# Kernel tuning notes

Hardware: AMD Instinct MI355X
Metric: run time of the kernel (lower is better)

The kernel has to match this reference:

```python
import jax, jax.numpy as jnp
import numpy as np

B, H, W = 4, 64, 64
INPLANES, PLANES, G, K = 608, 152, 19, 3
KK = K * K
EPS = 1e-5


def conv2d(x, w, stride=1, padding=0, dilation=1):
    return jax.lax.conv_general_dilated(
        x, w, (stride, stride), [(padding, padding)] * 2,
        rhs_dilation=(dilation, dilation),
        dimension_numbers=("NCHW", "OIHW", "NCHW"))


def bn(x, g, b, m, v):
    # inference-mode batchnorm (affine with running stats)
    inv = g / jnp.sqrt(v + EPS)
    return x * inv[None, :, None, None] + (b - m * inv)[None, :, None, None]


def deform_conv(x, offset, w, pad=1, dil=1):
    # x: [B,C,H,W], offset: [B, 2*G*KK, H, W] ((dy,dx) pairs per group per tap), w: [Cout,C,K,K]
    Bs, C, Hh, Ww = x.shape
    Cg = C // G
    off = offset.reshape(Bs, G, KK, 2, Hh, Ww)
    ky, kx = jnp.meshgrid(jnp.arange(K), jnp.arange(K), indexing="ij")
    base_y = (jnp.arange(Hh) - pad)[None, None, None, :, None] + (dil * ky.reshape(-1))[None, None, :, None, None]
    base_x = (jnp.arange(Ww) - pad)[None, None, None, None, :] + (dil * kx.reshape(-1))[None, None, :, None, None]
    ys = base_y + off[:, :, :, 0]  # [B,G,KK,H,W]
    xs = base_x + off[:, :, :, 1]
    y0 = jnp.floor(ys)
    x0 = jnp.floor(xs)
    wy = ys - y0
    wx = xs - x0
    y0i = y0.astype(jnp.int32)
    x0i = x0.astype(jnp.int32)
    xf = x.reshape(Bs, G, Cg, Hh * Ww)

    def gather(yi, xi, wgt):
        valid = ((yi >= 0) & (yi < Hh) & (xi >= 0) & (xi < Ww)).astype(x.dtype)
        idx = jnp.clip(yi, 0, Hh - 1) * Ww + jnp.clip(xi, 0, Ww - 1)
        idxf = jnp.broadcast_to(idx.reshape(Bs, G, 1, KK * Hh * Ww), (Bs, G, Cg, KK * Hh * Ww))
        g = jnp.take_along_axis(xf, idxf, axis=3).reshape(Bs, G, Cg, KK, Hh, Ww)
        return g * (wgt * valid)[:, :, None]

    samp = (gather(y0i, x0i, (1 - wy) * (1 - wx))
            + gather(y0i, x0i + 1, (1 - wy) * wx)
            + gather(y0i + 1, x0i, wy * (1 - wx))
            + gather(y0i + 1, x0i + 1, wy * wx))  # [B,G,Cg,KK,H,W]
    wr = w.reshape(w.shape[0], G, Cg, KK)
    return jnp.einsum("bgckhw,ogck->bohw", samp, wr)


def setup_inputs() -> dict:
    key = jax.random.key(0)
    ks = jax.random.split(key, 8)
    d = {}
    d["x"] = jax.random.normal(ks[0], (B, INPLANES, H, W), jnp.float32)
    d["conv1_w"] = jax.random.normal(ks[1], (PLANES, INPLANES, 1, 1), jnp.float32) * 0.05
    d["conv2_w"] = jax.random.normal(ks[2], (2 * G * KK, PLANES, 3, 3), jnp.float32) * 0.01
    d["dconv_w"] = jax.random.normal(ks[3], (PLANES, PLANES, 3, 3), jnp.float32) * 0.05
    d["conv3_w"] = jax.random.normal(ks[4], (4 * PLANES, PLANES, 1, 1), jnp.float32) * 0.05
    for i, (name, c) in enumerate([("bn1", PLANES), ("bn2", PLANES), ("bn3", 4 * PLANES)]):
        k1, k2, k3, k4 = jax.random.split(ks[5 + i], 4)
        d[name + "_g"] = jax.random.uniform(k1, (c,), jnp.float32, 0.5, 1.5)
        d[name + "_b"] = jax.random.normal(k2, (c,), jnp.float32) * 0.1
        d[name + "_m"] = jax.random.normal(k3, (c,), jnp.float32) * 0.1
        d[name + "_v"] = jax.random.uniform(k4, (c,), jnp.float32, 0.5, 1.5)
    return d


def reference(x, conv1_w, conv2_w, dconv_w, conv3_w,
              bn1_g, bn1_b, bn1_m, bn1_v,
              bn2_g, bn2_b, bn2_m, bn2_v,
              bn3_g, bn3_b, bn3_m, bn3_v):
    out = jax.nn.relu(conv2d(x, conv1_w))           # conv1 -> relu (order as in source)
    out = bn(out, bn1_g, bn1_b, bn1_m, bn1_v)       # -> bn1
    offset = conv2d(out, conv2_w, padding=1)         # offset-generating 3x3 conv
    out = deform_conv(out, offset, dconv_w)          # deformable 3x3 conv
    out = bn(jax.nn.relu(out), bn2_g, bn2_b, bn2_m, bn2_v)
    out = bn(conv2d(out, conv3_w), bn3_g, bn3_b, bn3_m, bn3_v)
    return jax.nn.relu(out + x)
```

## Files before the change

### kernel.cpp

```cpp
#include <hip/hip_runtime.h>

#define EPSV 1e-5f

typedef __bf16 bf16_t;
typedef __bf16 bf16x8 __attribute__((ext_vector_type(8)));
typedef float f32x4 __attribute__((ext_vector_type(4)));

__device__ inline bf16x8 bzero8() {
  bf16x8 z;
#pragma unroll
  for (int i = 0; i < 8; i++) z[i] = (bf16_t)0.f;
  return z;
}

__device__ inline f32x4 mfma16(bf16x8 a, bf16x8 b, f32x4 c) {
  return __builtin_amdgcn_mfma_f32_16x16x32_bf16(a, b, c, 0, 0, 0);
}

#define W1E (160 * 608)
#define W2E (384 * 1376)
#define WDE (192 * 1376)
#define W3E (640 * 160)

__global__ __launch_bounds__(256) void prep_weights(
    const float* __restrict__ w1, const float* __restrict__ w2,
    const float* __restrict__ wd, const float* __restrict__ w3,
    bf16_t* __restrict__ w1b, bf16_t* __restrict__ w2b,
    bf16_t* __restrict__ wdb, bf16_t* __restrict__ w3b) {
  int i = blockIdx.x * 256 + threadIdx.x;
  float v = 0.f;
  if (i < W1E) {
    int oc = i / 608, ic = i % 608;
    if (oc < 152) v = w1[oc * 608 + ic];
    w1b[i] = (bf16_t)v;
  } else if (i < W1E + W2E) {
    int j = i - W1E;
    int oc = j / 1376, k = j % 1376;
    if (oc < 342 && k < 1368) {
      int t = k / 152, ic = k % 152;
      v = w2[(oc * 152 + ic) * 9 + t];
    }
    w2b[j] = (bf16_t)v;
  } else if (i < W1E + W2E + WDE) {
    int j = i - W1E - W2E;
    int o = j / 1376, k = j % 1376;
    if (o < 152 && k < 1368) {
      int g = k / 72, r = k % 72, t = r / 8, cg = r % 8;
      v = wd[(o * 152 + g * 8 + cg) * 9 + t];
    }
    wdb[j] = (bf16_t)v;
  } else if (i < W1E + W2E + WDE + W3E) {
    int j = i - W1E - W2E - WDE;
    int oc = j / 160, ic = j % 160;
    if (oc < 608 && ic < 152) v = w3[oc * 152 + ic];
    w3b[j] = (bf16_t)v;
  }
}

__global__ void prep_bn(const float* g1, const float* b1, const float* m1, const float* v1,
                        const float* g2, const float* b2, const float* m2, const float* v2,
                        const float* g3, const float* b3, const float* m3, const float* v3,
                        float* __restrict__ bnc) {
  int i = threadIdx.x;
  if (i < 152) {
    float inv = g1[i] / sqrtf(v1[i] + EPSV);
    bnc[i] = inv;
    bnc[152 + i] = b1[i] - m1[i] * inv;
    float inv2 = g2[i] / sqrtf(v2[i] + EPSV);
    bnc[304 + i] = inv2;
    bnc[456 + i] = b2[i] - m2[i] * inv2;
  }
  if (i < 608) {
    float inv3 = g3[i] / sqrtf(v3[i] + EPSV);
    bnc[608 + i] = inv3;
    bnc[1216 + i] = b3[i] - m3[i] * inv3;
  }
}

__global__ __launch_bounds__(256) void s1_conv1(const float* __restrict__ x,
                                                const bf16_t* __restrict__ w1b,
                                                const float* __restrict__ bnc,
                                                bf16_t* __restrict__ out1) {
  __shared__ bf16_t t1[32 * 616];
  int tid = threadIdx.x;
  int px0 = blockIdx.x * 32;
  int b = px0 >> 12, sp0 = px0 & 4095;
  for (int task = tid; task < 608 * 2; task += 256) {
    int c = task >> 1, ch = task & 1;
    const float* src = x + (((size_t)(b * 608 + c)) << 12) + sp0 + ch * 16;
#pragma unroll
    for (int i = 0; i < 16; i++) t1[(ch * 16 + i) * 616 + c] = (bf16_t)src[i];
  }
  __syncthreads();
  int wid = tid >> 6, lane = tid & 63, q = lane >> 4, lr = lane & 15;
  int mw = wid & 1, nw = wid >> 1;
  f32x4 acc[5];
#pragma unroll
  for (int n = 0; n < 5; n++) acc[n] = (f32x4){0.f, 0.f, 0.f, 0.f};
  for (int kk = 0; kk < 19; kk++) {
    int k0 = kk * 32 + q * 8;
    bf16x8 a = *(const bf16x8*)(t1 + (mw * 16 + lr) * 616 + k0);
#pragma unroll
    for (int n = 0; n < 5; n++) {
      bf16x8 bf = *(const bf16x8*)(w1b + (nw * 80 + n * 16 + lr) * 608 + k0);
      acc[n] = mfma16(a, bf, acc[n]);
    }
  }
#pragma unroll
  for (int n = 0; n < 5; n++) {
    int oc = nw * 80 + n * 16 + lr;
    if (oc < 152) {
      float inv = bnc[oc], beta = bnc[152 + oc];
#pragma unroll
      for (int i = 0; i < 4; i++) {
        int p = px0 + mw * 16 + q * 4 + i;
        float v = fmaxf(acc[n][i], 0.f) * inv + beta;
        out1[(size_t)p * 152 + oc] = (bf16_t)v;
      }
    }
  }
}

__global__ __launch_bounds__(512) void s2_offs(const bf16_t* __restrict__ out1,
                                               const bf16_t* __restrict__ w2b,
                                               float* __restrict__ offs) {
  __shared__ bf16_t t2[102 * 152];
  int tid = threadIdx.x;
  int xh = blockIdx.x & 1, y = (blockIdx.x >> 1) & 63, b = blockIdx.x >> 7;
  const bf16_t* ob = out1 + (((size_t)b) << 12) * 152;
  int x0 = xh * 32 - 1;
  for (int task = tid; task < 3 * 34 * 19; task += 512) {
    int j = task / 646, r = task % 646;
    int xi = r / 19, cb = r % 19;
    int yy = y + j - 1, xx = x0 + xi;
    bf16x8 v = bzero8();
    if (yy >= 0 && yy < 64 && xx >= 0 && xx < 64)
      v = *(const bf16x8*)(ob + (size_t)(yy * 64 + xx) * 152 + cb * 8);
    *(bf16x8*)(t2 + (j * 34 + xi) * 152 + cb * 8) = v;
  }
  __syncthreads();
  int wid = tid >> 6, lane = tid & 63, q = lane >> 4, lr = lane & 15;
  f32x4 acc[2][3];
#pragma unroll
  for (int m = 0; m < 2; m++)
#pragma unroll
    for (int n = 0; n < 3; n++) acc[m][n] = (f32x4){0.f, 0.f, 0.f, 0.f};
  for (int kk = 0; kk < 43; kk++) {
    int k0 = kk * 32 + q * 8;
    bf16x8 a[2];
    if (k0 < 1368) {
      int t = k0 / 152, c0 = k0 - t * 152;
      int dy = t / 3, dxp1 = t - dy * 3;
      int base = (dy * 34 + lr + dxp1) * 152 + c0;
#pragma unroll
      for (int m = 0; m < 2; m++) a[m] = *(const bf16x8*)(t2 + base + m * 16 * 152);
    } else {
      a[0] = bzero8();
      a[1] = bzero8();
    }
#pragma unroll
    for (int n = 0; n < 3; n++) {
      bf16x8 bf = *(const bf16x8*)(w2b + (size_t)(wid * 48 + n * 16 + lr) * 1376 + k0);
#pragma unroll
      for (int m = 0; m < 2; m++) acc[m][n] = mfma16(a[m], bf, acc[m][n]);
    }
  }
#pragma unroll
  for (int n = 0; n < 3; n++) {
    int col = wid * 48 + n * 16 + lr;
    if (col < 342) {
#pragma unroll
      for (int m = 0; m < 2; m++)
#pragma unroll
        for (int i = 0; i < 4; i++) {
          int p = (b << 12) + y * 64 + xh * 32 + m * 16 + q * 4 + i;
          offs[(size_t)p * 344 + col] = acc[m][n][i];
        }
    }
  }
}

__global__ __launch_bounds__(256) void s3_dconv(const bf16_t* __restrict__ out1,
                                                const float* __restrict__ offs,
                                                const bf16_t* __restrict__ wdb,
                                                const float* __restrict__ bnc,
                                                bf16_t* __restrict__ a2) {
  __shared__ bf16_t alds[16 * 1368];
  int tid = threadIdx.x;
  int row0 = blockIdx.x * 16;
  for (int task = tid; task < 16 * 171; task += 256) {
    int r = task / 171, s = task % 171;
    int p = row0 + r;
    int b = p >> 12, y = (p >> 6) & 63, xc = p & 63;
    int g = s / 9, t = s % 9;
    const float* op = offs + (size_t)p * 344 + g * 18 + t * 2;
    float ys = (float)(y - 1 + t / 3) + op[0];
    float xs = (float)(xc - 1 + t % 3) + op[1];
    float y0f = floorf(ys), x0f = floorf(xs);
    float wy = ys - y0f, wx = xs - x0f;
    int y0 = (int)y0f, x0 = (int)x0f;
    float fa[8];
#pragma unroll
    for (int i = 0; i < 8; i++) fa[i] = 0.f;
    const bf16_t* base = out1 + (((size_t)b << 12) * 152) + g * 8;
    float ww0 = (1.f - wy) * (1.f - wx), ww1 = (1.f - wy) * wx;
    float ww2 = wy * (1.f - wx), ww3 = wy * wx;
    float wws[4] = {ww0, ww1, ww2, ww3};
    int yy[4] = {y0, y0, y0 + 1, y0 + 1};
    int xx[4] = {x0, x0 + 1, x0, x0 + 1};
#pragma unroll
    for (int cn = 0; cn < 4; cn++) {
      if (yy[cn] >= 0 && yy[cn] < 64 && xx[cn] >= 0 && xx[cn] < 64) {
        bf16x8 v = *(const bf16x8*)(base + (size_t)(yy[cn] * 64 + xx[cn]) * 152);
#pragma unroll
        for (int i = 0; i < 8; i++) fa[i] += wws[cn] * (float)v[i];
      }
    }
    bf16x8 o;
#pragma unroll
    for (int i = 0; i < 8; i++) o[i] = (bf16_t)fa[i];
    *(bf16x8*)(alds + r * 1368 + s * 8) = o;
  }
  __syncthreads();
  int wid = tid >> 6, lane = tid & 63, q = lane >> 4, lr = lane & 15;
  int nb = wid * 3;
  f32x4 acc[3];
#pragma unroll
  for (int n = 0; n < 3; n++) acc[n] = (f32x4){0.f, 0.f, 0.f, 0.f};
  for (int kk = 0; kk < 43; kk++) {
    int k0 = kk * 32 + q * 8;
    bf16x8 a = (k0 < 1368) ? *(const bf16x8*)(alds + lr * 1368 + k0) : bzero8();
#pragma unroll
    for (int n = 0; n < 3; n++) {
      bf16x8 bf = *(const bf16x8*)(wdb + (size_t)((nb + n) * 16 + lr) * 1376 + k0);
      acc[n] = mfma16(a, bf, acc[n]);
    }
  }
#pragma unroll
  for (int n = 0; n < 3; n++) {
    int oc = (nb + n) * 16 + lr;
    if (oc < 152) {
      float inv = bnc[304 + oc], beta = bnc[456 + oc];
#pragma unroll
      for (int i = 0; i < 4; i++) {
        int p = row0 + q * 4 + i;
        float v = fmaxf(acc[n][i], 0.f) * inv + beta;
        a2[(size_t)p * 152 + oc] = (bf16_t)v;
      }
    }
  }
}

__global__ __launch_bounds__(256) void s4_conv3(const bf16_t* __restrict__ a2,
                                                const bf16_t* __restrict__ w3b,
                                                const float* __restrict__ bnc,
                                                const float* __restrict__ x,
                                                float* __restrict__ out) {
  int tid = threadIdx.x;
  int wid = tid >> 6, lane = tid & 63, q = lane >> 4, lr = lane & 15;
  int p0 = blockIdx.x * 16;
  int b = p0 >> 12, sp0 = p0 & 4095;
  f32x4 acc[10];
#pragma unroll
  for (int n = 0; n < 10; n++) acc[n] = (f32x4){0.f, 0.f, 0.f, 0.f};
  for (int kk = 0; kk < 5; kk++) {
    int k0 = kk * 32 + q * 8;
    bf16x8 a = (k0 < 152) ? *(const bf16x8*)(a2 + (size_t)(p0 + lr) * 152 + k0) : bzero8();
#pragma unroll
    for (int n = 0; n < 10; n++) {
      bf16x8 bf = *(const bf16x8*)(w3b + (size_t)(wid * 160 + n * 16 + lr) * 160 + k0);
      acc[n] = mfma16(a, bf, acc[n]);
    }
  }
#pragma unroll
  for (int n = 0; n < 10; n++) {
    int oc = wid * 160 + n * 16 + lr;
    if (oc < 608) {
      float inv = bnc[608 + oc], beta = bnc[1216 + oc];
      size_t gi = (((size_t)(b * 608 + oc)) << 12) + sp0 + q * 4;
      f32x4 xr = *(const f32x4*)(x + gi);
      f32x4 o;
#pragma unroll
      for (int i = 0; i < 4; i++) o[i] = fmaxf(acc[n][i] * inv + beta + xr[i], 0.f);
      *(f32x4*)(out + gi) = o;
    }
  }
}

extern "C" void kernel_launch(void* const* d_in, const int* in_sizes, int n_in,
                              void* d_out, int out_size, void* d_ws, size_t ws_size,
                              hipStream_t stream) {
  const float* x = (const float*)d_in[0];
  const float* w1 = (const float*)d_in[1];
  const float* w2 = (const float*)d_in[2];
  const float* wd = (const float*)d_in[3];
  const float* w3 = (const float*)d_in[4];
  const float* g1 = (const float*)d_in[5];
  const float* b1 = (const float*)d_in[6];
  const float* m1 = (const float*)d_in[7];
  const float* v1 = (const float*)d_in[8];
  const float* g2 = (const float*)d_in[9];
  const float* b2 = (const float*)d_in[10];
  const float* m2 = (const float*)d_in[11];
  const float* v2 = (const float*)d_in[12];
  const float* g3 = (const float*)d_in[13];
  const float* b3 = (const float*)d_in[14];
  const float* m3 = (const float*)d_in[15];
  const float* v3 = (const float*)d_in[16];

  char* ws = (char*)d_ws;
  bf16_t* w1b = (bf16_t*)(ws + 0);
  bf16_t* w2b = (bf16_t*)(ws + 194560);
  bf16_t* wdb = (bf16_t*)(ws + 1251328);
  bf16_t* w3b = (bf16_t*)(ws + 1779712);
  float* bnc = (float*)(ws + 1984512);
  bf16_t* out1 = (bf16_t*)(ws + 1991808);
  float* offs = (float*)(ws + 6972544);
  bf16_t* a2 = (bf16_t*)(ws + 29516928);
  float* out = (float*)d_out;

  prep_weights<<<3876, 256, 0, stream>>>(w1, w2, wd, w3, w1b, w2b, wdb, w3b);
  prep_bn<<<1, 640, 0, stream>>>(g1, b1, m1, v1, g2, b2, m2, v2, g3, b3, m3, v3, bnc);
  s1_conv1<<<512, 256, 0, stream>>>(x, w1b, bnc, out1);
  s2_offs<<<512, 512, 0, stream>>>(out1, w2b, offs);
  s3_dconv<<<1024, 256, 0, stream>>>(out1, offs, wdb, bnc, a2);
  s4_conv3<<<1024, 256, 0, stream>>>(a2, w3b, bnc, x, out);
}
```

Baseline: 180.9 us.

## Reorder offset and deform-weight layout tap-major and remap dconv sampling threads

Offsets are now written tap-major (t*38+g*2+c) and the deform-conv weights are reordered to match (k = t*152+ic). In the sampling phase each of 171 threads owns one (tap, group) pair and loops over 16 pixels, reading offsets as a float2. The sampled tile is stored in the matching tap-major LDS layout. The conv1 input transpose now uses float4 vector loads, and dconv gets a launch bound of 3 blocks per CU. The remap is meant to make offset reads and neighbouring gathers more coalesced, but it leaves only 171 of 256 threads active during sampling and serializes 16 pixels per thread.

Result: slower. 202.7 us (+12.1%).

```diff
diff --git a/kernel.cpp b/kernel.cpp
--- a/kernel.cpp
+++ b/kernel.cpp
@@ -45,8 +45,8 @@
     int j = i - W1E - W2E;
     int o = j / 1376, k = j % 1376;
     if (o < 152 && k < 1368) {
-      int g = k / 72, r = k % 72, t = r / 8, cg = r % 8;
-      v = wd[(o * 152 + g * 8 + cg) * 9 + t];
+      int t = k / 152, ic = k % 152;
+      v = wd[(o * 152 + ic) * 9 + t];
     }
     wdb[j] = (bf16_t)v;
   } else if (i < W1E + W2E + WDE + W3E) {
@@ -85,11 +85,11 @@
   int tid = threadIdx.x;
   int px0 = blockIdx.x * 32;
   int b = px0 >> 12, sp0 = px0 & 4095;
-  for (int task = tid; task < 608 * 2; task += 256) {
-    int c = task >> 1, ch = task & 1;
-    const float* src = x + (((size_t)(b * 608 + c)) << 12) + sp0 + ch * 16;
-#pragma unroll
-    for (int i = 0; i < 16; i++) t1[(ch * 16 + i) * 616 + c] = (bf16_t)src[i];
+  for (int task = tid; task < 608 * 8; task += 256) {
+    int c = task >> 3, i4 = task & 7;
+    f32x4 v = *(const f32x4*)(x + (((size_t)(b * 608 + c)) << 12) + sp0 + i4 * 4);
+#pragma unroll
+    for (int i = 0; i < 4; i++) t1[(i4 * 4 + i) * 616 + c] = (bf16_t)v[i];
   }
   __syncthreads();
   int wid = tid >> 6, lane = tid & 63, q = lane >> 4, lr = lane & 15;
@@ -169,57 +169,65 @@
   for (int n = 0; n < 3; n++) {
     int col = wid * 48 + n * 16 + lr;
     if (col < 342) {
+      int g = col / 18, rem = col % 18;
+      int t = rem >> 1, c = rem & 1;
+      int pos = t * 38 + g * 2 + c;
 #pragma unroll
       for (int m = 0; m < 2; m++)
 #pragma unroll
         for (int i = 0; i < 4; i++) {
           int p = (b << 12) + y * 64 + xh * 32 + m * 16 + q * 4 + i;
-          offs[(size_t)p * 344 + col] = acc[m][n][i];
+          offs[(size_t)p * 344 + pos] = acc[m][n][i];
         }
     }
   }
 }
 
-__global__ __launch_bounds__(256) void s3_dconv(const bf16_t* __restrict__ out1,
-                                                const float* __restrict__ offs,
-                                                const bf16_t* __restrict__ wdb,
-                                                const float* __restrict__ bnc,
-                                                bf16_t* __restrict__ a2) {
+__global__ __launch_bounds__(256, 3) void s3_dconv(const bf16_t* __restrict__ out1,
+                                                   const float* __restrict__ offs,
+                                                   const bf16_t* __restrict__ wdb,
+                                                   const float* __restrict__ bnc,
+                                                   bf16_t* __restrict__ a2) {
   __shared__ bf16_t alds[16 * 1368];
   int tid = threadIdx.x;
   int row0 = blockIdx.x * 16;
-  for (int task = tid; task < 16 * 171; task += 256) {
-    int r = task / 171, s = task % 171;
-    int p = row0 + r;
-    int b = p >> 12, y = (p >> 6) & 63, xc = p & 63;
-    int g = s / 9, t = s % 9;
-    const float* op = offs + (size_t)p * 344 + g * 18 + t * 2;
-    float ys = (float)(y - 1 + t / 3) + op[0];
-    float xs = (float)(xc - 1 + t % 3) + op[1];
-    float y0f = floorf(ys), x0f = floorf(xs);
-    float wy = ys - y0f, wx = xs - x0f;
-    int y0 = (int)y0f, x0 = (int)x0f;
-    float fa[8];
-#pragma unroll
-    for (int i = 0; i < 8; i++) fa[i] = 0.f;
-    const bf16_t* base = out1 + (((size_t)b << 12) * 152) + g * 8;
-    float ww0 = (1.f - wy) * (1.f - wx), ww1 = (1.f - wy) * wx;
-    float ww2 = wy * (1.f - wx), ww3 = wy * wx;
-    float wws[4] = {ww0, ww1, ww2, ww3};
-    int yy[4] = {y0, y0, y0 + 1, y0 + 1};
-    int xx[4] = {x0, x0 + 1, x0, x0 + 1};
-#pragma unroll
-    for (int cn = 0; cn < 4; cn++) {
-      if (yy[cn] >= 0 && yy[cn] < 64 && xx[cn] >= 0 && xx[cn] < 64) {
-        bf16x8 v = *(const bf16x8*)(base + (size_t)(yy[cn] * 64 + xx[cn]) * 152);
-#pragma unroll
-        for (int i = 0; i < 8; i++) fa[i] += wws[cn] * (float)v[i];
+  if (tid < 171) {
+    int t = tid / 19, g = tid - t * 19;
+    int ky = t / 3, kx = t - ky * 3;
+    int bb = row0 >> 12;
+    const bf16_t* base = out1 + (((size_t)bb << 12) * 152) + g * 8;
+    const float* op0 = offs + (size_t)row0 * 344 + t * 38 + g * 2;
+    bf16_t* ldst = alds + t * 152 + g * 8;
+#pragma unroll
+    for (int r = 0; r < 16; r++) {
+      int p = row0 + r;
+      int y = (p >> 6) & 63, xc = p & 63;
+      float2 ov = *(const float2*)(op0 + (size_t)r * 344);
+      float ys = (float)(y - 1 + ky) + ov.x;
+      float xs = (float)(xc - 1 + kx) + ov.y;
+      float y0f = floorf(ys), x0f = floorf(xs);
+      float wy = ys - y0f, wx = xs - x0f;
+      int y0 = (int)y0f, x0 = (int)x0f;
+      float fa[8];
+#pragma unroll
+      for (int i = 0; i < 8; i++) fa[i] = 0.f;
+      float wws[4] = {(1.f - wy) * (1.f - wx), (1.f - wy) * wx,
+                      wy * (1.f - wx), wy * wx};
+      int yy[4] = {y0, y0, y0 + 1, y0 + 1};
+      int xx[4] = {x0, x0 + 1, x0, x0 + 1};
+#pragma unroll
+      for (int cn = 0; cn < 4; cn++) {
+        if (yy[cn] >= 0 && yy[cn] < 64 && xx[cn] >= 0 && xx[cn] < 64) {
+          bf16x8 v = *(const bf16x8*)(base + (size_t)(yy[cn] * 64 + xx[cn]) * 152);
+#pragma unroll
+          for (int i = 0; i < 8; i++) fa[i] += wws[cn] * (float)v[i];
+        }
       }
-    }
-    bf16x8 o;
-#pragma unroll
-    for (int i = 0; i < 8; i++) o[i] = (bf16_t)fa[i];
-    *(bf16x8*)(alds + r * 1368 + s * 8) = o;
+      bf16x8 o;
+#pragma unroll
+      for (int i = 0; i < 8; i++) o[i] = (bf16_t)fa[i];
+      *(bf16x8*)(ldst + r * 1368) = o;
+    }
   }
   __syncthreads();
   int wid = tid >> 6, lane = tid & 63, q = lane >> 4, lr = lane & 15;
```
